# Optimization experiments

Measured on AMD Instinct MI355X. Metric: run time of the kernel, lower is better.

The kernel has to match this reference:

```python
import jax, jax.numpy as jnp
import numpy as np

N_EXPERTS = 8
Z_DIM = 128
HID = 1024
OUT = 3072  # e.g. 3x32x32 flattened generator output
BATCH = 2048


def hash_vectors(z, n):
    """Deterministic per-sample hash -> expert index in [0, n).

    Proxy for the repo's hash_vectors (which hashes the latent vector):
    quantize |z|, sum over feature dim, mod n. Non-differentiable by design.
    """
    return jnp.mod(jnp.floor(jnp.abs(z) * 1000.0).sum(axis=1).astype(jnp.int32), n)


def setup_inputs() -> dict:
    key = jax.random.key(0)
    kz, k1, kb1, k2, kb2 = jax.random.split(key, 5)
    z = jax.random.normal(kz, (BATCH, Z_DIM), dtype=jnp.float32)
    s1 = 1.0 / np.sqrt(Z_DIM)
    s2 = 1.0 / np.sqrt(HID)
    # Stacked per-expert MLP params (each expert independently initialized,
    # mirroring reset_parameters on each deepcopy).
    W1 = jax.random.uniform(k1, (N_EXPERTS, Z_DIM, HID), jnp.float32, -s1, s1)
    b1 = jax.random.uniform(kb1, (N_EXPERTS, HID), jnp.float32, -s1, s1)
    W2 = jax.random.uniform(k2, (N_EXPERTS, HID, OUT), jnp.float32, -s2, s2)
    b2 = jax.random.uniform(kb2, (N_EXPERTS, OUT), jnp.float32, -s2, s2)
    return {"z": z, "W1": W1, "b1": b1, "W2": W2, "b2": b2}


def reference(z, W1, b1, W2, b2):
    # Hard routing: each sample i goes to expert idx[i].
    idx = hash_vectors(z, N_EXPERTS)  # [B]
    # Dense compute-all-experts then select (vectorized replacement for the
    # per-sample Python loop in the original forward).
    h = jax.nn.relu(jnp.einsum('bi,eih->beh', z, W1) + b1[None, :, :])  # [B,E,H]
    y = jnp.einsum('beh,eho->beo', h, W2) + b2[None, :, :]              # [B,E,O]
    out = jnp.take_along_axis(y, idx[:, None, None], axis=1)[:, 0, :]   # [B,O]
    return out
```

## Files before the change

### kernel.cpp

```cpp
#include <hip/hip_runtime.h>
#include <hip/hip_bf16.h>


#define BATCH 2048
#define ZD 128
#define HID 1024
#define OUTD 3072
#define NEXP 8

#define TMG 128
#define TNG 128
#define BKG 64
#define MAXTF 24

#define TM 64
#define TN 32

typedef short bf16x8 __attribute__((ext_vector_type(8)));
typedef float f32x4 __attribute__((ext_vector_type(4)));


__global__ __launch_bounds__(256) void route_kernel(const float* __restrict__ z,
                                                    int* counts, int* bucket) {
    int gid = blockIdx.x * 256 + threadIdx.x;
    int s_idx = gid >> 6;
    int lane = gid & 63;
    float a = z[s_idx * ZD + lane];
    float b = z[s_idx * ZD + 64 + lane];
    float s = floorf(fabsf(a) * 1000.0f) + floorf(fabsf(b) * 1000.0f);
#pragma unroll
    for (int off = 32; off > 0; off >>= 1) s += __shfl_down(s, off);
    if (lane == 0) {
        int e = ((int)s) & 7;
        int pos = atomicAdd(&counts[e], 1);
        bucket[e * BATCH + pos] = s_idx;
    }
}

__global__ void scan_kernel(const int* __restrict__ counts, int* ntl,
                            int* tstart, int* tcnt, int* texp, int* perm,
                            const int* __restrict__ bucket, int TMv) {
    __shared__ int soff[NEXP + 1];
    __shared__ int scnt[NEXP];
    if (threadIdx.x == 0) {
        int o = 0;
        for (int e = 0; e < NEXP; e++) {
            scnt[e] = counts[e];
            soff[e] = o;
            tstart[e] = o / TMv;
            int t = (scnt[e] + TMv - 1) / TMv;
            tcnt[e] = t;
            o += t * TMv;
        }
        soff[NEXP] = o;
        *ntl = o / TMv;
    }
    __syncthreads();
    int total = soff[NEXP];
    for (int r = threadIdx.x; r < total; r += blockDim.x) {
        int e = 0;
        while (r >= soff[e + 1]) e++;
        int i = r - soff[e];
        perm[r] = (i < scnt[e]) ? bucket[e * BATCH + i] : -1;
        if (r % TMv == 0) texp[r / TMv] = e;
    }
}

__global__ __launch_bounds__(256) void convz_kernel(const float* __restrict__ z,
                                                    __hip_bfloat16* __restrict__ zb) {
    int idx = blockIdx.x * 256 + threadIdx.x;
    float4 v = ((const float4*)z)[idx];
    union { uint2 u; __hip_bfloat16 h[4]; } o;
    o.h[0] = __float2bfloat16(v.x);
    o.h[1] = __float2bfloat16(v.y);
    o.h[2] = __float2bfloat16(v.z);
    o.h[3] = __float2bfloat16(v.w);
    ((uint2*)zb)[idx] = o.u;
}

__global__ __launch_bounds__(256) void trans_kernel(const float* __restrict__ W,
                                                    __hip_bfloat16* __restrict__ WT,
                                                    int K, int N) {
    int e = blockIdx.z;
    int n0 = blockIdx.x * 64;
    int k0 = blockIdx.y * 64;
    const float* Wp = W + (size_t)e * K * N;
    __hip_bfloat16* Op = WT + (size_t)e * N * K;
    __shared__ __hip_bfloat16 Ts[64][68];
    int t = threadIdx.x;
    int kk = t >> 4, nn = (t & 15) * 4;
#pragma unroll
    for (int i = 0; i < 4; i++) {
        int k = i * 16 + kk;
        float4 v = *(const float4*)(Wp + (size_t)(k0 + k) * N + n0 + nn);
        Ts[k][nn + 0] = __float2bfloat16(v.x);
        Ts[k][nn + 1] = __float2bfloat16(v.y);
        Ts[k][nn + 2] = __float2bfloat16(v.z);
        Ts[k][nn + 3] = __float2bfloat16(v.w);
    }
    __syncthreads();
    int n = t >> 2;
#pragma unroll
    for (int p = 0; p < 2; p++) {
        int ch = p * 4 + (t & 3);
        union { bf16x8 v; __hip_bfloat16 h[8]; } u;
#pragma unroll
        for (int j = 0; j < 8; j++) u.h[j] = Ts[ch * 8 + j][n];
        *(bf16x8*)(Op + (size_t)(n0 + n) * K + k0 + ch * 8) = u.v;
    }
}


__global__ __launch_bounds__(256, 3) void gemm1_fast(
    const __hip_bfloat16* __restrict__ zb, const __hip_bfloat16* __restrict__ W1T,
    const float* __restrict__ b1, const int* __restrict__ ntl,
    const int* __restrict__ texp, const int* __restrict__ perm,
    __hip_bfloat16* __restrict__ H) {
    int mt = blockIdx.y;
    if (mt >= *ntl) return;
    int e = texp[mt];
    int n0 = blockIdx.x * TNG;

    __shared__ __align__(16) __hip_bfloat16 As[TMG * BKG];
    __shared__ __align__(16) __hip_bfloat16 Bs[TNG * BKG];
    __shared__ int rows_s[TMG];

    int tid = threadIdx.x;
    if (tid < TMG) rows_s[tid] = perm[mt * TMG + tid];
    __syncthreads();

    int lane = tid & 63, wave = tid >> 6;
    int cc = lane & 15, q = lane >> 4;
    int mw = (wave >> 1) * 64, nw = (wave & 1) * 64;

    int sr = tid >> 3, sc = tid & 7;
    int wbase = sr * 64 + (sc ^ (sr & 7)) * 8;
    const __hip_bfloat16* Bg = W1T + ((size_t)e * HID + n0 + sr) * ZD + sc * 8;
    const __hip_bfloat16* Arp[4];
#pragma unroll
    for (int p = 0; p < 4; p++) {
        int r = rows_s[p * 32 + sr];
        if (r < 0) r = 0;
        Arp[p] = zb + (size_t)r * ZD + sc * 8;
    }

    int A0 = (mw + cc) * 64, B0 = (nw + cc) * 64;
    int X0 = (q ^ (cc & 7)) * 8, X1 = ((4 + q) ^ (cc & 7)) * 8;

    float bias[4];
#pragma unroll
    for (int j = 0; j < 4; j++) bias[j] = b1[(size_t)e * HID + n0 + nw + j * 16 + cc];

    f32x4 zero4 = {0.f, 0.f, 0.f, 0.f};
    f32x4 acc[4][4];
#pragma unroll
    for (int i = 0; i < 4; i++)
#pragma unroll
        for (int j = 0; j < 4; j++) acc[i][j] = zero4;

    bf16x8 ga[4], gb[4];
#pragma unroll
    for (int p = 0; p < 4; p++) {
        ga[p] = *(const bf16x8*)(Arp[p]);
        gb[p] = *(const bf16x8*)(Bg + (size_t)p * 32 * ZD);
    }
#pragma unroll
    for (int it = 0; it < ZD / BKG; ++it) {
        __syncthreads();
#pragma unroll
        for (int p = 0; p < 4; p++) {
            *(bf16x8*)(As + wbase + p * 2048) = ga[p];
            *(bf16x8*)(Bs + wbase + p * 2048) = gb[p];
        }
        __syncthreads();
        if (it + 1 < ZD / BKG) {
#pragma unroll
            for (int p = 0; p < 4; p++) {
                ga[p] = *(const bf16x8*)(Arp[p] + (it + 1) * BKG);
                gb[p] = *(const bf16x8*)(Bg + (size_t)p * 32 * ZD + (it + 1) * BKG);
            }
        }
#pragma unroll
        for (int kh = 0; kh < 2; ++kh) {
            int X = kh ? X1 : X0;
            bf16x8 af[4], bfr[4];
#pragma unroll
            for (int i = 0; i < 4; i++) af[i] = *(const bf16x8*)(As + A0 + i * 1024 + X);
#pragma unroll
            for (int j = 0; j < 4; j++) bfr[j] = *(const bf16x8*)(Bs + B0 + j * 1024 + X);
#pragma unroll
            for (int i = 0; i < 4; i++)
#pragma unroll
                for (int j = 0; j < 4; j++)
                    acc[i][j] = __builtin_amdgcn_mfma_f32_16x16x32_bf16(af[i], bfr[j],
                                                                        acc[i][j], 0, 0, 0);
        }
    }
#pragma unroll
    for (int i = 0; i < 4; i++)
#pragma unroll
        for (int r = 0; r < 4; r++) {
            int m = mw + i * 16 + q * 4 + r;
            __hip_bfloat16* hp = H + (size_t)(mt * TMG + m) * HID + n0 + nw + cc;
#pragma unroll
            for (int j = 0; j < 4; j++)
                hp[j * 16] = __float2bfloat16(fmaxf(acc[i][j][r] + bias[j], 0.f));
        }
}

__global__ __launch_bounds__(256, 3) void gemm2_fast(
    const __hip_bfloat16* __restrict__ H, const __hip_bfloat16* __restrict__ W2T,
    const float* __restrict__ b2, const int* __restrict__ ntl,
    const int* __restrict__ texp, const int* __restrict__ perm,
    float* __restrict__ out) {
    int mt = blockIdx.y;
    if (mt >= *ntl) return;
    int e = texp[mt];
    int n0 = blockIdx.x * TNG;

    __shared__ __align__(16) __hip_bfloat16 As[TMG * BKG];
    __shared__ __align__(16) __hip_bfloat16 Bs[TNG * BKG];
    __shared__ int rows_s[TMG];

    int tid = threadIdx.x;
    if (tid < TMG) rows_s[tid] = perm[mt * TMG + tid];

    int lane = tid & 63, wave = tid >> 6;
    int cc = lane & 15, q = lane >> 4;
    int mw = (wave >> 1) * 64, nw = (wave & 1) * 64;

    int sr = tid >> 3, sc = tid & 7;
    int wbase = sr * 64 + (sc ^ (sr & 7)) * 8;
    const __hip_bfloat16* Ag = H + ((size_t)mt * TMG + sr) * HID + sc * 8;
    const __hip_bfloat16* Bg = W2T + ((size_t)e * OUTD + n0 + sr) * HID + sc * 8;

    int A0 = (mw + cc) * 64, B0 = (nw + cc) * 64;
    int X0 = (q ^ (cc & 7)) * 8, X1 = ((4 + q) ^ (cc & 7)) * 8;

    float bias[4];
#pragma unroll
    for (int j = 0; j < 4; j++) bias[j] = b2[(size_t)e * OUTD + n0 + nw + j * 16 + cc];

    f32x4 zero4 = {0.f, 0.f, 0.f, 0.f};
    f32x4 acc[4][4];
#pragma unroll
    for (int i = 0; i < 4; i++)
#pragma unroll
        for (int j = 0; j < 4; j++) acc[i][j] = zero4;

    bf16x8 ga[4], gb[4];
#pragma unroll
    for (int p = 0; p < 4; p++) {
        ga[p] = *(const bf16x8*)(Ag + (size_t)p * 32 * HID);
        gb[p] = *(const bf16x8*)(Bg + (size_t)p * 32 * HID);
    }
    for (int it = 0; it < HID / BKG; ++it) {
        __syncthreads();
#pragma unroll
        for (int p = 0; p < 4; p++) {
            *(bf16x8*)(As + wbase + p * 2048) = ga[p];
            *(bf16x8*)(Bs + wbase + p * 2048) = gb[p];
        }
        __syncthreads();
        if (it + 1 < HID / BKG) {
            int k1 = (it + 1) * BKG;
#pragma unroll
            for (int p = 0; p < 4; p++) {
                ga[p] = *(const bf16x8*)(Ag + (size_t)p * 32 * HID + k1);
                gb[p] = *(const bf16x8*)(Bg + (size_t)p * 32 * HID + k1);
            }
        }
#pragma unroll
        for (int kh = 0; kh < 2; ++kh) {
            int X = kh ? X1 : X0;
            bf16x8 af[4], bfr[4];
#pragma unroll
            for (int i = 0; i < 4; i++) af[i] = *(const bf16x8*)(As + A0 + i * 1024 + X);
#pragma unroll
            for (int j = 0; j < 4; j++) bfr[j] = *(const bf16x8*)(Bs + B0 + j * 1024 + X);
#pragma unroll
            for (int i = 0; i < 4; i++)
#pragma unroll
                for (int j = 0; j < 4; j++)
                    acc[i][j] = __builtin_amdgcn_mfma_f32_16x16x32_bf16(af[i], bfr[j],
                                                                        acc[i][j], 0, 0, 0);
        }
    }
#pragma unroll
    for (int i = 0; i < 4; i++)
#pragma unroll
        for (int r = 0; r < 4; r++) {
            int m = mw + i * 16 + q * 4 + r;
            int orow = rows_s[m];
            if (orow >= 0) {
                float* op = out + (size_t)orow * OUTD + n0 + nw + cc;
#pragma unroll
                for (int j = 0; j < 4; j++) op[j * 16] = acc[i][j][r] + bias[j];
            }
        }
}

__global__ __launch_bounds__(256, 2) void gemm1_fb(
    const float* __restrict__ z, const float* __restrict__ W1,
    const float* __restrict__ b1, const int* __restrict__ tstart,
    const int* __restrict__ tcnt, const int* __restrict__ perm,
    __hip_bfloat16* __restrict__ H) {
    int e = blockIdx.y;
    int tc = tcnt[e];
    if (tc == 0) return;
    int ts = tstart[e];
    int n0 = blockIdx.x * TN;
    __shared__ __align__(16) __hip_bfloat16 Bs[(ZD / 8) * TN * 8];
    __shared__ int rows_s[TM];
    int tid = threadIdx.x;
    const float* W = W1 + (size_t)e * ZD * HID;
#pragma unroll
    for (int i = 0; i < 2; ++i) {
        int ko = i * 8 + (tid >> 5);
        int n = tid & 31;
        union { bf16x8 v8; __hip_bfloat16 h[8]; } u;
#pragma unroll
        for (int j = 0; j < 8; ++j)
            u.h[j] = __float2bfloat16(W[(size_t)(ko * 8 + j) * HID + n0 + n]);
        *(bf16x8*)((char*)Bs + (size_t)(ko * TN + n) * 16) = u.v8;
    }
    int lane = tid & 63, wave = tid >> 6;
    int mw = wave * 16;
    int cc = lane & 15, q = lane >> 4;
    float bias0 = b1[(size_t)e * HID + n0 + cc];
    float bias1 = b1[(size_t)e * HID + n0 + 16 + cc];
    __syncthreads();
    for (int mi = 0; mi < tc; ++mi) {
        int mt = ts + mi;
        __syncthreads();
        if (tid < TM) rows_s[tid] = perm[mt * TM + tid];
        __syncthreads();
        int arow = rows_s[mw + cc];
        const float* zp = z + (size_t)(arow < 0 ? 0 : arow) * ZD + q * 8;
        f32x4 acc0 = {0.f, 0.f, 0.f, 0.f}, acc1 = acc0;
#pragma unroll
        for (int s = 0; s < ZD / 32; ++s) {
            float4 v0 = ((const float4*)(zp + s * 32))[0];
            float4 v1 = ((const float4*)(zp + s * 32))[1];
            float v[8] = {v0.x, v0.y, v0.z, v0.w, v1.x, v1.y, v1.z, v1.w};
            union { bf16x8 v8; __hip_bfloat16 h[8]; } u;
#pragma unroll
            for (int j = 0; j < 8; ++j)
                u.h[j] = __float2bfloat16(arow < 0 ? 0.f : v[j]);
            bf16x8 b0 = *(const bf16x8*)((char*)Bs + (size_t)((s * 4 + q) * TN + cc) * 16);
            bf16x8 b1v = *(const bf16x8*)((char*)Bs + (size_t)((s * 4 + q) * TN + 16 + cc) * 16);
            acc0 = __builtin_amdgcn_mfma_f32_16x16x32_bf16(u.v8, b0, acc0, 0, 0, 0);
            acc1 = __builtin_amdgcn_mfma_f32_16x16x32_bf16(u.v8, b1v, acc1, 0, 0, 0);
        }
#pragma unroll
        for (int r = 0; r < 4; ++r) {
            int m = mw + q * 4 + r;
            size_t hb = (size_t)(mt * TM + m) * HID + n0;
            H[hb + cc] = __float2bfloat16(fmaxf(acc0[r] + bias0, 0.f));
            H[hb + 16 + cc] = __float2bfloat16(fmaxf(acc1[r] + bias1, 0.f));
        }
    }
}

__global__ __launch_bounds__(256, 2) void gemm2_fb(
    const __hip_bfloat16* __restrict__ H, const float* __restrict__ W2,
    const float* __restrict__ b2, const int* __restrict__ tstart,
    const int* __restrict__ tcnt, const int* __restrict__ perm,
    float* __restrict__ out) {
    int e = blockIdx.y;
    int tc = tcnt[e];
    if (tc == 0) return;
    int ts = tstart[e];
    int n0 = blockIdx.x * TN;
    __shared__ __align__(16) __hip_bfloat16 Bs[(HID / 8) * TN * 8];
    __shared__ int rows_s[TM];
    int tid = threadIdx.x;
    const float* W = W2 + (size_t)e * HID * OUTD;
#pragma unroll 4
    for (int i = 0; i < 16; ++i) {
        int ko = i * 8 + (tid >> 5);
        int n = tid & 31;
        union { bf16x8 v8; __hip_bfloat16 h[8]; } u;
#pragma unroll
        for (int j = 0; j < 8; ++j)
            u.h[j] = __float2bfloat16(W[(size_t)(ko * 8 + j) * OUTD + n0 + n]);
        *(bf16x8*)((char*)Bs + (size_t)(ko * TN + n) * 16) = u.v8;
    }
    int lane = tid & 63, wave = tid >> 6;
    int mw = wave * 16;
    int cc = lane & 15, q = lane >> 4;
    float bias0 = b2[(size_t)e * OUTD + n0 + cc];
    float bias1 = b2[(size_t)e * OUTD + n0 + 16 + cc];
    __syncthreads();
    for (int mi = 0; mi < tc; ++mi) {
        int mt = ts + mi;
        __syncthreads();
        if (tid < TM) rows_s[tid] = perm[mt * TM + tid];
        __syncthreads();
        const __hip_bfloat16* Ab = H + (size_t)(mt * TM + mw + cc) * HID + q * 8;
        f32x4 acc0 = {0.f, 0.f, 0.f, 0.f}, acc1 = acc0;
#pragma unroll 8
        for (int s = 0; s < HID / 32; ++s) {
            bf16x8 af = *(const bf16x8*)(Ab + s * 32);
            bf16x8 b0 = *(const bf16x8*)((char*)Bs + (size_t)((s * 4 + q) * TN + cc) * 16);
            bf16x8 b1v = *(const bf16x8*)((char*)Bs + (size_t)((s * 4 + q) * TN + 16 + cc) * 16);
            acc0 = __builtin_amdgcn_mfma_f32_16x16x32_bf16(af, b0, acc0, 0, 0, 0);
            acc1 = __builtin_amdgcn_mfma_f32_16x16x32_bf16(af, b1v, acc1, 0, 0, 0);
        }
#pragma unroll
        for (int r = 0; r < 4; ++r) {
            int m = mw + q * 4 + r;
            int orow = rows_s[m];
            if (orow >= 0) {
                size_t ob = (size_t)orow * OUTD + n0;
                out[ob + cc] = acc0[r] + bias0;
                out[ob + 16 + cc] = acc1[r] + bias1;
            }
        }
    }
}

extern "C" void kernel_launch(void* const* d_in, const int* in_sizes, int n_in,
                              void* d_out, int out_size, void* d_ws, size_t ws_size,
                              hipStream_t stream) {
    const float* z  = (const float*)d_in[0];
    const float* W1 = (const float*)d_in[1];
    const float* b1 = (const float*)d_in[2];
    const float* W2 = (const float*)d_in[3];
    const float* b2 = (const float*)d_in[4];
    float* out = (float*)d_out;

    char* ws = (char*)d_ws;
    int* counts = (int*)ws;
    int* ntl    = (int*)(ws + 64);
    int* tstart = (int*)(ws + 128);
    int* tcnt   = (int*)(ws + 192);
    int* texp   = (int*)(ws + 256);
    int* perm   = (int*)(ws + 512);

    const size_t NEED = 59322880ull;
    hipMemsetAsync(counts, 0, 64, stream);

    if (ws_size >= NEED) {
        int* bucket = (int*)(ws + 12800);
        __hip_bfloat16* zb  = (__hip_bfloat16*)(ws + 78336);
        __hip_bfloat16* Hb  = (__hip_bfloat16*)(ws + 602624);
        __hip_bfloat16* W1T = (__hip_bfloat16*)(ws + 6894080);
        __hip_bfloat16* W2T = (__hip_bfloat16*)(ws + 8991232);

        hipLaunchKernelGGL(route_kernel, dim3(BATCH / 4), dim3(256), 0, stream,
                           z, counts, bucket);
        hipLaunchKernelGGL(scan_kernel, dim3(1), dim3(256), 0, stream,
                           counts, ntl, tstart, tcnt, texp, perm, bucket, TMG);
        hipLaunchKernelGGL(convz_kernel, dim3(BATCH * ZD / 1024), dim3(256), 0, stream,
                           z, zb);
        hipLaunchKernelGGL(trans_kernel, dim3(HID / 64, ZD / 64, NEXP), dim3(256), 0,
                           stream, W1, W1T, ZD, HID);
        hipLaunchKernelGGL(trans_kernel, dim3(OUTD / 64, HID / 64, NEXP), dim3(256), 0,
                           stream, W2, W2T, HID, OUTD);
        hipLaunchKernelGGL(gemm1_fast, dim3(HID / TNG, MAXTF), dim3(256), 0, stream,
                           zb, W1T, b1, ntl, texp, perm, Hb);
        hipLaunchKernelGGL(gemm2_fast, dim3(OUTD / TNG, MAXTF), dim3(256), 0, stream,
                           Hb, W2T, b2, ntl, texp, perm, out);
    } else {
        int* bucket = (int*)(ws + 10752);
        __hip_bfloat16* Hb = (__hip_bfloat16*)(ws + 76288);

        hipLaunchKernelGGL(route_kernel, dim3(BATCH / 4), dim3(256), 0, stream,
                           z, counts, bucket);
        hipLaunchKernelGGL(scan_kernel, dim3(1), dim3(256), 0, stream,
                           counts, ntl, tstart, tcnt, texp, perm, bucket, TM);
        hipLaunchKernelGGL(gemm1_fb, dim3(HID / TN, NEXP), dim3(256), 0, stream,
                           z, W1, b1, tstart, tcnt, perm, Hb);
        hipLaunchKernelGGL(gemm2_fb, dim3(OUTD / TN, NEXP), dim3(256), 0, stream,
                           Hb, W2, b2, tstart, tcnt, perm, out);
    }
}
```

Measured before the change: 236.7 us.

## Fuse z conversion into routing and widen swizzled weight transpose tiles

```diff
diff --git a/kernel.cpp b/kernel.cpp
--- a/kernel.cpp
+++ b/kernel.cpp
@@ -13,33 +13,55 @@
 #define BKG 64
 #define MAXTF 24
 
-#define TM 64
-#define TN 32
-
 typedef short bf16x8 __attribute__((ext_vector_type(8)));
 typedef float f32x4 __attribute__((ext_vector_type(4)));
 
 
 __global__ __launch_bounds__(256) void route_kernel(const float* __restrict__ z,
+                                                    __hip_bfloat16* __restrict__ zb,
                                                     int* counts, int* bucket) {
-    int gid = blockIdx.x * 256 + threadIdx.x;
-    int s_idx = gid >> 6;
-    int lane = gid & 63;
-    float a = z[s_idx * ZD + lane];
-    float b = z[s_idx * ZD + 64 + lane];
-    float s = floorf(fabsf(a) * 1000.0f) + floorf(fabsf(b) * 1000.0f);
-#pragma unroll
-    for (int off = 32; off > 0; off >>= 1) s += __shfl_down(s, off);
-    if (lane == 0) {
-        int e = ((int)s) & 7;
-        int pos = atomicAdd(&counts[e], 1);
-        bucket[e * BATCH + pos] = s_idx;
-    }
+    __shared__ int lcnt[NEXP];
+    __shared__ int gbase[NEXP];
+    int t = threadIdx.x;
+    if (t < NEXP) lcnt[t] = 0;
+    __syncthreads();
+
+    int s = blockIdx.x * 32 + (t >> 3);
+    int li = t & 7;
+    const float* zp = z + (size_t)s * ZD + li * 16;
+    float sum = 0.f;
+    union { bf16x8 v8; __hip_bfloat16 h[8]; } u0, u1;
+#pragma unroll
+    for (int i = 0; i < 4; i++) {
+        float4 v = ((const float4*)zp)[i];
+        sum += floorf(fabsf(v.x) * 1000.0f) + floorf(fabsf(v.y) * 1000.0f) +
+               floorf(fabsf(v.z) * 1000.0f) + floorf(fabsf(v.w) * 1000.0f);
+        __hip_bfloat16* dst = (i < 2) ? &u0.h[i * 4] : &u1.h[(i - 2) * 4];
+        dst[0] = __float2bfloat16(v.x);
+        dst[1] = __float2bfloat16(v.y);
+        dst[2] = __float2bfloat16(v.z);
+        dst[3] = __float2bfloat16(v.w);
+    }
+    bf16x8* zo = (bf16x8*)(zb + (size_t)s * ZD + li * 16);
+    zo[0] = u0.v8;
+    zo[1] = u1.v8;
+
+    sum += __shfl_down(sum, 4);
+    sum += __shfl_down(sum, 2);
+    sum += __shfl_down(sum, 1);
+    int e = 0, lpos = 0;
+    if (li == 0) {
+        e = ((int)sum) & 7;
+        lpos = atomicAdd(&lcnt[e], 1);
+    }
+    __syncthreads();
+    if (t < NEXP) gbase[t] = atomicAdd(&counts[t], lcnt[t]);
+    __syncthreads();
+    if (li == 0) bucket[e * BATCH + gbase[e] + lpos] = s;
 }
 
 __global__ void scan_kernel(const int* __restrict__ counts, int* ntl,
-                            int* tstart, int* tcnt, int* texp, int* perm,
-                            const int* __restrict__ bucket, int TMv) {
+                            int* texp, int* perm, const int* __restrict__ bucket) {
     __shared__ int soff[NEXP + 1];
     __shared__ int scnt[NEXP];
     if (threadIdx.x == 0) {
@@ -47,13 +69,10 @@
         for (int e = 0; e < NEXP; e++) {
             scnt[e] = counts[e];
             soff[e] = o;
-            tstart[e] = o / TMv;
-            int t = (scnt[e] + TMv - 1) / TMv;
-            tcnt[e] = t;
-            o += t * TMv;
+            o += (scnt[e] + TMG - 1) & ~(TMG - 1);
         }
         soff[NEXP] = o;
-        *ntl = o / TMv;
+        *ntl = o / TMG;
     }
     __syncthreads();
     int total = soff[NEXP];
@@ -62,20 +81,8 @@
         while (r >= soff[e + 1]) e++;
         int i = r - soff[e];
         perm[r] = (i < scnt[e]) ? bucket[e * BATCH + i] : -1;
-        if (r % TMv == 0) texp[r / TMv] = e;
-    }
-}
-
-__global__ __launch_bounds__(256) void convz_kernel(const float* __restrict__ z,
-                                                    __hip_bfloat16* __restrict__ zb) {
-    int idx = blockIdx.x * 256 + threadIdx.x;
-    float4 v = ((const float4*)z)[idx];
-    union { uint2 u; __hip_bfloat16 h[4]; } o;
-    o.h[0] = __float2bfloat16(v.x);
-    o.h[1] = __float2bfloat16(v.y);
-    o.h[2] = __float2bfloat16(v.z);
-    o.h[3] = __float2bfloat16(v.w);
-    ((uint2*)zb)[idx] = o.u;
+        if ((r & (TMG - 1)) == 0) texp[r / TMG] = e;
+    }
 }
 
 __global__ __launch_bounds__(256) void trans_kernel(const float* __restrict__ W,
@@ -83,30 +90,38 @@
                                                     int K, int N) {
     int e = blockIdx.z;
     int n0 = blockIdx.x * 64;
-    int k0 = blockIdx.y * 64;
+    int k0 = blockIdx.y * 128;
     const float* Wp = W + (size_t)e * K * N;
     __hip_bfloat16* Op = WT + (size_t)e * N * K;
-    __shared__ __hip_bfloat16 Ts[64][68];
+    __shared__ __align__(16) __hip_bfloat16 Ts[64 * 16 * 8];
+
     int t = threadIdx.x;
-    int kk = t >> 4, nn = (t & 15) * 4;
-#pragma unroll
-    for (int i = 0; i < 4; i++) {
-        int k = i * 16 + kk;
-        float4 v = *(const float4*)(Wp + (size_t)(k0 + k) * N + n0 + nn);
-        Ts[k][nn + 0] = __float2bfloat16(v.x);
-        Ts[k][nn + 1] = __float2bfloat16(v.y);
-        Ts[k][nn + 2] = __float2bfloat16(v.z);
-        Ts[k][nn + 3] = __float2bfloat16(v.w);
-    }
-    __syncthreads();
+    int nn = (t & 15) * 4;
+    int kb = (t >> 4) * 8;
+    int c = t >> 4;
+
+    float4 v[8];
+#pragma unroll
+    for (int i = 0; i < 8; i++)
+        v[i] = *(const float4*)(Wp + (size_t)(k0 + kb + i) * N + n0 + nn);
+
+#pragma unroll
+    for (int j = 0; j < 4; j++) {
+        union { bf16x8 v8; __hip_bfloat16 h[8]; } u;
+        float* f = (float*)v;
+#pragma unroll
+        for (int i = 0; i < 8; i++) u.h[i] = __float2bfloat16(f[i * 4 + j]);
+        int n = nn + j;
+        *(bf16x8*)(Ts + ((size_t)n * 16 + (c ^ (n & 7))) * 8) = u.v8;
+    }
+    __syncthreads();
+
     int n = t >> 2;
 #pragma unroll
-    for (int p = 0; p < 2; p++) {
-        int ch = p * 4 + (t & 3);
-        union { bf16x8 v; __hip_bfloat16 h[8]; } u;
-#pragma unroll
-        for (int j = 0; j < 8; j++) u.h[j] = Ts[ch * 8 + j][n];
-        *(bf16x8*)(Op + (size_t)(n0 + n) * K + k0 + ch * 8) = u.v;
+    for (int p = 0; p < 4; p++) {
+        int cd = p * 4 + (t & 3);
+        bf16x8 val = *(const bf16x8*)(Ts + ((size_t)n * 16 + (cd ^ (n & 7))) * 8);
+        *(bf16x8*)(Op + (size_t)(n0 + n) * K + k0 + cd * 8) = val;
     }
 }
 
@@ -300,126 +315,6 @@
         }
 }
 
-__global__ __launch_bounds__(256, 2) void gemm1_fb(
-    const float* __restrict__ z, const float* __restrict__ W1,
-    const float* __restrict__ b1, const int* __restrict__ tstart,
-    const int* __restrict__ tcnt, const int* __restrict__ perm,
-    __hip_bfloat16* __restrict__ H) {
-    int e = blockIdx.y;
-    int tc = tcnt[e];
-    if (tc == 0) return;
-    int ts = tstart[e];
-    int n0 = blockIdx.x * TN;
-    __shared__ __align__(16) __hip_bfloat16 Bs[(ZD / 8) * TN * 8];
-    __shared__ int rows_s[TM];
-    int tid = threadIdx.x;
-    const float* W = W1 + (size_t)e * ZD * HID;
-#pragma unroll
-    for (int i = 0; i < 2; ++i) {
-        int ko = i * 8 + (tid >> 5);
-        int n = tid & 31;
-        union { bf16x8 v8; __hip_bfloat16 h[8]; } u;
-#pragma unroll
-        for (int j = 0; j < 8; ++j)
-            u.h[j] = __float2bfloat16(W[(size_t)(ko * 8 + j) * HID + n0 + n]);
-        *(bf16x8*)((char*)Bs + (size_t)(ko * TN + n) * 16) = u.v8;
-    }
-    int lane = tid & 63, wave = tid >> 6;
-    int mw = wave * 16;
-    int cc = lane & 15, q = lane >> 4;
-    float bias0 = b1[(size_t)e * HID + n0 + cc];
-    float bias1 = b1[(size_t)e * HID + n0 + 16 + cc];
-    __syncthreads();
-    for (int mi = 0; mi < tc; ++mi) {
-        int mt = ts + mi;
-        __syncthreads();
-        if (tid < TM) rows_s[tid] = perm[mt * TM + tid];
-        __syncthreads();
-        int arow = rows_s[mw + cc];
-        const float* zp = z + (size_t)(arow < 0 ? 0 : arow) * ZD + q * 8;
-        f32x4 acc0 = {0.f, 0.f, 0.f, 0.f}, acc1 = acc0;
-#pragma unroll
-        for (int s = 0; s < ZD / 32; ++s) {
-            float4 v0 = ((const float4*)(zp + s * 32))[0];
-            float4 v1 = ((const float4*)(zp + s * 32))[1];
-            float v[8] = {v0.x, v0.y, v0.z, v0.w, v1.x, v1.y, v1.z, v1.w};
-            union { bf16x8 v8; __hip_bfloat16 h[8]; } u;
-#pragma unroll
-            for (int j = 0; j < 8; ++j)
-                u.h[j] = __float2bfloat16(arow < 0 ? 0.f : v[j]);
-            bf16x8 b0 = *(const bf16x8*)((char*)Bs + (size_t)((s * 4 + q) * TN + cc) * 16);
-            bf16x8 b1v = *(const bf16x8*)((char*)Bs + (size_t)((s * 4 + q) * TN + 16 + cc) * 16);
-            acc0 = __builtin_amdgcn_mfma_f32_16x16x32_bf16(u.v8, b0, acc0, 0, 0, 0);
-            acc1 = __builtin_amdgcn_mfma_f32_16x16x32_bf16(u.v8, b1v, acc1, 0, 0, 0);
-        }
-#pragma unroll
-        for (int r = 0; r < 4; ++r) {
-            int m = mw + q * 4 + r;
-            size_t hb = (size_t)(mt * TM + m) * HID + n0;
-            H[hb + cc] = __float2bfloat16(fmaxf(acc0[r] + bias0, 0.f));
-            H[hb + 16 + cc] = __float2bfloat16(fmaxf(acc1[r] + bias1, 0.f));
-        }
-    }
-}
-
-__global__ __launch_bounds__(256, 2) void gemm2_fb(
-    const __hip_bfloat16* __restrict__ H, const float* __restrict__ W2,
-    const float* __restrict__ b2, const int* __restrict__ tstart,
-    const int* __restrict__ tcnt, const int* __restrict__ perm,
-    float* __restrict__ out) {
-    int e = blockIdx.y;
-    int tc = tcnt[e];
-    if (tc == 0) return;
-    int ts = tstart[e];
-    int n0 = blockIdx.x * TN;
-    __shared__ __align__(16) __hip_bfloat16 Bs[(HID / 8) * TN * 8];
-    __shared__ int rows_s[TM];
-    int tid = threadIdx.x;
-    const float* W = W2 + (size_t)e * HID * OUTD;
-#pragma unroll 4
-    for (int i = 0; i < 16; ++i) {
-        int ko = i * 8 + (tid >> 5);
-        int n = tid & 31;
-        union { bf16x8 v8; __hip_bfloat16 h[8]; } u;
-#pragma unroll
-        for (int j = 0; j < 8; ++j)
-            u.h[j] = __float2bfloat16(W[(size_t)(ko * 8 + j) * OUTD + n0 + n]);
-        *(bf16x8*)((char*)Bs + (size_t)(ko * TN + n) * 16) = u.v8;
-    }
-    int lane = tid & 63, wave = tid >> 6;
-    int mw = wave * 16;
-    int cc = lane & 15, q = lane >> 4;
-    float bias0 = b2[(size_t)e * OUTD + n0 + cc];
-    float bias1 = b2[(size_t)e * OUTD + n0 + 16 + cc];
-    __syncthreads();
-    for (int mi = 0; mi < tc; ++mi) {
-        int mt = ts + mi;
-        __syncthreads();
-        if (tid < TM) rows_s[tid] = perm[mt * TM + tid];
-        __syncthreads();
-        const __hip_bfloat16* Ab = H + (size_t)(mt * TM + mw + cc) * HID + q * 8;
-        f32x4 acc0 = {0.f, 0.f, 0.f, 0.f}, acc1 = acc0;
-#pragma unroll 8
-        for (int s = 0; s < HID / 32; ++s) {
-            bf16x8 af = *(const bf16x8*)(Ab + s * 32);
-            bf16x8 b0 = *(const bf16x8*)((char*)Bs + (size_t)((s * 4 + q) * TN + cc) * 16);
-            bf16x8 b1v = *(const bf16x8*)((char*)Bs + (size_t)((s * 4 + q) * TN + 16 + cc) * 16);
-            acc0 = __builtin_amdgcn_mfma_f32_16x16x32_bf16(af, b0, acc0, 0, 0, 0);
-            acc1 = __builtin_amdgcn_mfma_f32_16x16x32_bf16(af, b1v, acc1, 0, 0, 0);
-        }
-#pragma unroll
-        for (int r = 0; r < 4; ++r) {
-            int m = mw + q * 4 + r;
-            int orow = rows_s[m];
-            if (orow >= 0) {
-                size_t ob = (size_t)orow * OUTD + n0;
-                out[ob + cc] = acc0[r] + bias0;
-                out[ob + 16 + cc] = acc1[r] + bias1;
-            }
-        }
-    }
-}
-
 extern "C" void kernel_launch(void* const* d_in, const int* in_sizes, int n_in,
                               void* d_out, int out_size, void* d_ws, size_t ws_size,
                               hipStream_t stream) {
@@ -433,46 +328,25 @@
     char* ws = (char*)d_ws;
     int* counts = (int*)ws;
     int* ntl    = (int*)(ws + 64);
-    int* tstart = (int*)(ws + 128);
-    int* tcnt   = (int*)(ws + 192);
-    int* texp   = (int*)(ws + 256);
-    int* perm   = (int*)(ws + 512);
-
-    const size_t NEED = 59322880ull;
+    int* texp   = (int*)(ws + 128);
+    int* perm   = (int*)(ws + 256);
+    int* bucket = (int*)(ws + 12544);
+    __hip_bfloat16* zb  = (__hip_bfloat16*)(ws + 78080);
+    __hip_bfloat16* Hb  = (__hip_bfloat16*)(ws + 602368);
+    __hip_bfloat16* W1T = (__hip_bfloat16*)(ws + 6893824);
+    __hip_bfloat16* W2T = (__hip_bfloat16*)(ws + 8990976);
+
     hipMemsetAsync(counts, 0, 64, stream);
-
-    if (ws_size >= NEED) {
-        int* bucket = (int*)(ws + 12800);
-        __hip_bfloat16* zb  = (__hip_bfloat16*)(ws + 78336);
-        __hip_bfloat16* Hb  = (__hip_bfloat16*)(ws + 602624);
-        __hip_bfloat16* W1T = (__hip_bfloat16*)(ws + 6894080);
-        __hip_bfloat16* W2T = (__hip_bfloat16*)(ws + 8991232);
-
-        hipLaunchKernelGGL(route_kernel, dim3(BATCH / 4), dim3(256), 0, stream,
-                           z, counts, bucket);
-        hipLaunchKernelGGL(scan_kernel, dim3(1), dim3(256), 0, stream,
-                           counts, ntl, tstart, tcnt, texp, perm, bucket, TMG);
-        hipLaunchKernelGGL(convz_kernel, dim3(BATCH * ZD / 1024), dim3(256), 0, stream,
-                           z, zb);
-        hipLaunchKernelGGL(trans_kernel, dim3(HID / 64, ZD / 64, NEXP), dim3(256), 0,
-                           stream, W1, W1T, ZD, HID);
-        hipLaunchKernelGGL(trans_kernel, dim3(OUTD / 64, HID / 64, NEXP), dim3(256), 0,
-                           stream, W2, W2T, HID, OUTD);
-        hipLaunchKernelGGL(gemm1_fast, dim3(HID / TNG, MAXTF), dim3(256), 0, stream,
-                           zb, W1T, b1, ntl, texp, perm, Hb);
-        hipLaunchKernelGGL(gemm2_fast, dim3(OUTD / TNG, MAXTF), dim3(256), 0, stream,
-                           Hb, W2T, b2, ntl, texp, perm, out);
-    } else {
-        int* bucket = (int*)(ws + 10752);
-        __hip_bfloat16* Hb = (__hip_bfloat16*)(ws + 76288);
-
-        hipLaunchKernelGGL(route_kernel, dim3(BATCH / 4), dim3(256), 0, stream,
-                           z, counts, bucket);
-        hipLaunchKernelGGL(scan_kernel, dim3(1), dim3(256), 0, stream,
-                           counts, ntl, tstart, tcnt, texp, perm, bucket, TM);
-        hipLaunchKernelGGL(gemm1_fb, dim3(HID / TN, NEXP), dim3(256), 0, stream,
-                           z, W1, b1, tstart, tcnt, perm, Hb);
-        hipLaunchKernelGGL(gemm2_fb, dim3(OUTD / TN, NEXP), dim3(256), 0, stream,
-                           Hb, W2, b2, tstart, tcnt, perm, out);
-    }
-}
+    hipLaunchKernelGGL(route_kernel, dim3(BATCH / 32), dim3(256), 0, stream,
+                       z, zb, counts, bucket);
+    hipLaunchKernelGGL(scan_kernel, dim3(1), dim3(256), 0, stream,
+                       counts, ntl, texp, perm, bucket);
+    hipLaunchKernelGGL(trans_kernel, dim3(HID / 64, ZD / 128, NEXP), dim3(256), 0,
+                       stream, W1, W1T, ZD, HID);
+    hipLaunchKernelGGL(trans_kernel, dim3(OUTD / 64, HID / 128, NEXP), dim3(256), 0,
+                       stream, W2, W2T, HID, OUTD);
+    hipLaunchKernelGGL(gemm1_fast, dim3(HID / TNG, MAXTF), dim3(256), 0, stream,
+                       zb, W1T, b1, ntl, texp, perm, Hb);
+    hipLaunchKernelGGL(gemm2_fast, dim3(OUTD / TNG, MAXTF), dim3(256), 0, stream,
+                       Hb, W2T, b2, ntl, texp, perm, out);
+}
```

Result: faster. 215.3 us (-9.0%).
